# Kernel optimization log

Measured on AMD Instinct MI355X. Metric: run time of the kernel, lower is better.

Reference implementation:

```python
import jax, jax.numpy as jnp
import numpy as np

N_TYPES = 6
NUM_HEADS = 8
MAX_SEQ = 50
LN_EPS = 1e-5
NEG_SLOPE = 0.2


def layer_norm(x, g, b):
    m = x.mean(-1, keepdims=True)
    v = ((x - m) ** 2).mean(-1, keepdims=True)
    return (x - m) / jnp.sqrt(v + LN_EPS) * g + b


def setup_inputs() -> dict:
    key = jax.random.key(0)
    N, E, D = 20000, 200000, 128  # nodes, edges, input_dim==hidden_dim
    ks = jax.random.split(key, 64)
    it = iter(ks)

    def w(shape):
        return jax.random.normal(next(it), shape, jnp.float32) / np.sqrt(shape[-2] if len(shape) > 1 else shape[-1]).astype(np.float32)

    inp = {}
    inp['x'] = jax.random.normal(next(it), (N, D), jnp.float32)
    inp['edge_index'] = jax.random.randint(next(it), (2, E), 0, N)
    inp['node_types'] = jax.random.randint(next(it), (N,), 0, N_TYPES)
    inp['temporal_positions'] = jax.random.randint(next(it), (N,), 0, MAX_SEQ)
    # CrossDomainGAT params
    inp['gat_Wq'] = w((D, D)); inp['gat_Wk'] = w((D, D)); inp['gat_Wv'] = w((D, D))
    inp['gat_Wo'] = w((D, D)); inp['gat_bo'] = jnp.zeros((D,), jnp.float32)
    inp['gat_g'] = jnp.ones((D,), jnp.float32); inp['gat_b'] = jnp.zeros((D,), jnp.float32)
    # SchemaAwareGCN params
    inp['gcn_Wt'] = w((N_TYPES, D, D)); inp['gcn_bt'] = jnp.zeros((N_TYPES, D), jnp.float32)
    inp['gcn_mW1'] = w((2 * D, D)); inp['gcn_mb1'] = jnp.zeros((D,), jnp.float32)
    inp['gcn_mW2'] = w((D, D)); inp['gcn_mb2'] = jnp.zeros((D,), jnp.float32)
    inp['gcn_aW1'] = w((D, D)); inp['gcn_ab1'] = jnp.zeros((D,), jnp.float32)
    inp['gcn_aW2'] = w((D, D)); inp['gcn_ab2'] = jnp.zeros((D,), jnp.float32)
    inp['gcn_Wo'] = w((D, D)); inp['gcn_bo'] = jnp.zeros((D,), jnp.float32)
    inp['gcn_g'] = jnp.ones((D,), jnp.float32); inp['gcn_b'] = jnp.zeros((D,), jnp.float32)
    # TemporalReasoningGNN params (no turn_boundaries -> LSTM/attention path skipped)
    inp['tmp_emb'] = jax.random.normal(next(it), (MAX_SEQ, D), jnp.float32)
    inp['tmp_W1'] = w((2 * D, D)); inp['tmp_b1'] = jnp.zeros((D,), jnp.float32)
    inp['tmp_W2'] = w((D, D)); inp['tmp_b2'] = jnp.zeros((D,), jnp.float32)
    inp['tmp_Wo'] = w((D, D)); inp['tmp_bo'] = jnp.zeros((D,), jnp.float32)
    inp['tmp_g'] = jnp.ones((D,), jnp.float32); inp['tmp_b'] = jnp.zeros((D,), jnp.float32)
    # Unified fusion (concat of 3 branches -> hidden) + LayerNorm
    inp['fus_W'] = w((3 * D, D)); inp['fus_b'] = jnp.zeros((D,), jnp.float32)
    inp['fus_g'] = jnp.ones((D,), jnp.float32); inp['fus_be'] = jnp.zeros((D,), jnp.float32)
    return inp


def _gat(x, row, col, Wq, Wk, Wv, Wo, bo, g, b):
    N, D = x.shape
    Dh = D // NUM_HEADS
    Q = (x @ Wq).reshape(N, NUM_HEADS, Dh)
    K = (x @ Wk).reshape(N, NUM_HEADS, Dh)
    V = (x @ Wv).reshape(N, NUM_HEADS, Dh)
    # edge-wise multi-head attention scores [E, H]
    scores = (Q[row] * K[col]).sum(-1) / np.sqrt(Dh).astype(np.float32)
    scores = jax.nn.leaky_relu(scores, NEG_SLOPE)
    # segment softmax over incoming edges of each col node
    mx = jax.ops.segment_max(scores, col, num_segments=N)
    ex = jnp.exp(scores - mx[col])
    sm = jax.ops.segment_sum(ex, col, num_segments=N)
    probs = ex / sm[col]
    wv = probs[:, :, None] * V[row]  # [E, H, Dh]
    out = jax.ops.segment_sum(wv.reshape(len(row), D), col, num_segments=N)
    out = out @ Wo + bo
    return layer_norm(out + x, g, b)


def _mlp2(z, W1, b1, W2, b2):
    return jax.nn.relu(z @ W1 + b1) @ W2 + b2


def _gcn(x, row, col, node_types, Wt, bt, mW1, mb1, mW2, mb2, aW1, ab1, aW2, ab2, Wo, bo, g, b):
    N, D = x.shape
    h = jnp.zeros((N, D), x.dtype)
    for t in range(N_TYPES):  # fixed small type count
        h = h + jnp.where((node_types == t)[:, None], x @ Wt[t] + bt[t], 0.0)
    messages = _mlp2(jnp.concatenate([h[row], h[col]], axis=1), mW1, mb1, mW2, mb2)
    agg = jax.ops.segment_sum(messages, col, num_segments=N)
    h = h + _mlp2(agg, aW1, ab1, aW2, ab2)
    h = h @ Wo + bo
    return layer_norm(h + x, g, b)


def _temporal(x, row, col, tpos, emb, W1, b1, W2, b2, Wo, bo, g, b):
    N, D = x.shape
    h = x + emb[jnp.clip(tpos, 0, MAX_SEQ - 1)]
    messages = _mlp2(jnp.concatenate([h[row], h[col]], axis=1), W1, b1, W2, b2)
    h = h + jax.ops.segment_sum(messages, col, num_segments=N)
    h = h @ Wo + bo
    return layer_norm(h, g, b)


def reference(x, edge_index, node_types, temporal_positions,
              gat_Wq, gat_Wk, gat_Wv, gat_Wo, gat_bo, gat_g, gat_b,
              gcn_Wt, gcn_bt, gcn_mW1, gcn_mb1, gcn_mW2, gcn_mb2,
              gcn_aW1, gcn_ab1, gcn_aW2, gcn_ab2, gcn_Wo, gcn_bo, gcn_g, gcn_b,
              tmp_emb, tmp_W1, tmp_b1, tmp_W2, tmp_b2, tmp_Wo, tmp_bo, tmp_g, tmp_b,
              fus_W, fus_b, fus_g, fus_be):
    row, col = edge_index[0], edge_index[1]
    o_gat = _gat(x, row, col, gat_Wq, gat_Wk, gat_Wv, gat_Wo, gat_bo, gat_g, gat_b)
    o_gcn = _gcn(x, row, col, node_types, gcn_Wt, gcn_bt, gcn_mW1, gcn_mb1, gcn_mW2, gcn_mb2,
                 gcn_aW1, gcn_ab1, gcn_aW2, gcn_ab2, gcn_Wo, gcn_bo, gcn_g, gcn_b)
    o_tmp = _temporal(x, row, col, temporal_positions, tmp_emb, tmp_W1, tmp_b1, tmp_W2, tmp_b2,
                      tmp_Wo, tmp_bo, tmp_g, tmp_b)
    fused = jnp.concatenate([o_gat, o_gcn, o_tmp], axis=-1) @ fus_W + fus_b
    return layer_norm(fused, fus_g, fus_be)
```

## Files before the change

kernel.cpp:

```cpp
#include <hip/hip_runtime.h>

using u32 = unsigned int;
using s64 = long long;

__global__ __launch_bounds__(64) void k_detect13(const u32* __restrict__ ei,
                                                 const u32* __restrict__ nt,
                                                 const u32* __restrict__ tp,
                                                 u32* __restrict__ flags) {
    if (blockIdx.x != 0 || threadIdx.x != 0) return;
    bool e64 = true, n64 = true, t64 = true;
    for (int k = 0; k < 64; ++k) {
        if (ei[2 * k + 1] != 0u) e64 = false;
        if (nt[2 * k + 1] != 0u) n64 = false;
        if (tp[2 * k + 1] != 0u) t64 = false;
    }
    flags[0] = e64 ? 1u : 0u;
    flags[1] = n64 ? 1u : 0u;
    flags[2] = t64 ? 1u : 0u;
}

__global__ __launch_bounds__(256) void k_cvt13(const void* __restrict__ src,
                                               int* __restrict__ dst, long long n,
                                               const u32* __restrict__ flags, int fidx) {
    long long i = (long long)blockIdx.x * 256 + threadIdx.x;
    if (i >= n) return;
    dst[i] = flags[fidx] ? (int)((const s64*)src)[i] : ((const int*)src)[i];
}

__global__ __launch_bounds__(256) void kz13(float* __restrict__ p, long long n) {
    long long i = (long long)blockIdx.x * 256 + threadIdx.x;
    if (i < n) p[i] = 0.f;
}
__global__ __launch_bounds__(256) void kz_i(int* __restrict__ p, int n) {
    int i = blockIdx.x * 256 + threadIdx.x;
    if (i < n) p[i] = 0;
}

__global__ __launch_bounds__(256) void k_hist(const int* __restrict__ ei, int E,
                                              int* __restrict__ cnt) {
    int e = blockIdx.x * 256 + threadIdx.x;
    if (e < E) atomicAdd(&cnt[ei[E + e]], 1);
}

__global__ __launch_bounds__(1024) void k_scan(const int* __restrict__ cnt,
                                               int* __restrict__ offA, int N) {
    __shared__ int part[1024];
    int t = threadIdx.x;
    int C = (N + 1023) >> 10;
    int beg = t * C, end = beg + C; if (end > N) end = N;
    int s = 0;
    for (int k = beg; k < end; ++k) s += cnt[k];
    part[t] = s; __syncthreads();
    for (int o = 1; o < 1024; o <<= 1) {
        int v = (t >= o) ? part[t - o] : 0;
        __syncthreads();
        part[t] += v;
        __syncthreads();
    }
    int base = (t == 0) ? 0 : part[t - 1];
    for (int k = beg; k < end; ++k) { offA[k] = base; base += cnt[k]; }
    if (t == 1023) offA[N] = part[1023];
}

__global__ __launch_bounds__(256) void k_scatter(const int* __restrict__ ei, int E,
                                                 const int* __restrict__ offA,
                                                 int* __restrict__ cur,
                                                 int* __restrict__ srow,
                                                 int* __restrict__ sedge) {
    int e = blockIdx.x * 256 + threadIdx.x;
    if (e >= E) return;
    int col = ei[E + e];
    int p = offA[col] + atomicAdd(&cur[col], 1);
    srow[p] = ei[e];
    sedge[p] = e;
}

__global__ __launch_bounds__(256) void k_thist(const int* __restrict__ nt, int N,
                                               int* __restrict__ tcnt) {
    __shared__ int lc[6];
    if (threadIdx.x < 6) lc[threadIdx.x] = 0;
    __syncthreads();
    int i = blockIdx.x * 256 + threadIdx.x;
    if (i < N) {
        int t = nt[i]; t = (t < 0 || t > 5) ? 0 : t;
        atomicAdd(&lc[t], 1);
    }
    __syncthreads();
    if (threadIdx.x < 6 && lc[threadIdx.x] > 0) atomicAdd(&tcnt[threadIdx.x], lc[threadIdx.x]);
}

__global__ __launch_bounds__(64) void k_tscan(const int* __restrict__ tcnt,
                                              int* __restrict__ toff) {
    if (threadIdx.x != 0 || blockIdx.x != 0) return;
    int s = 0;
    for (int t = 0; t < 6; ++t) { toff[t] = s; s += tcnt[t]; }
    toff[6] = s;
}

__global__ __launch_bounds__(256) void k_tscatter(const int* __restrict__ nt, int N,
                                                  const int* __restrict__ toff,
                                                  int* __restrict__ tcur,
                                                  int* __restrict__ perm) {
    __shared__ int lc[6], gb[6];
    if (threadIdx.x < 6) lc[threadIdx.x] = 0;
    __syncthreads();
    int i = blockIdx.x * 256 + threadIdx.x;
    int t = 0, lr = 0;
    if (i < N) {
        t = nt[i]; t = (t < 0 || t > 5) ? 0 : t;
        lr = atomicAdd(&lc[t], 1);
    }
    __syncthreads();
    if (threadIdx.x < 6 && lc[threadIdx.x] > 0)
        gb[threadIdx.x] = atomicAdd(&tcur[threadIdx.x], lc[threadIdx.x]);
    __syncthreads();
    if (i < N) perm[toff[t] + gb[t] + lr] = i;
}

__device__ __forceinline__ float2 ld2(const float* p) { return *(const float2*)p; }
__device__ __forceinline__ void st2(float* p, float2 v) { *(float2*)p = v; }
__device__ __forceinline__ float4 ld4(const float* p) { return *(const float4*)p; }
__device__ __forceinline__ void st4(float* p, float4 v) { *(float4*)p = v; }
__device__ __forceinline__ void fma4(float4& a, float s, float4 w) {
    a.x = fmaf(s, w.x, a.x); a.y = fmaf(s, w.y, a.y);
    a.z = fmaf(s, w.z, a.z); a.w = fmaf(s, w.w, a.w);
}

__device__ __forceinline__ float redrow(float s) {
#pragma unroll
    for (int o = 1; o < 32; o <<= 1) s += __shfl_xor(s, o);
    return s;
}


__device__ __forceinline__ void stage_half(float* wl, const float* __restrict__ Wg,
                                           int half) {
    int t = threadIdx.x;
    const float* src = Wg + half * 8192;
#pragma unroll
    for (int i = 0; i < 8; ++i) {
        int idx = (t + i * 256) * 4;
        st4(wl + idx, ld4(src + idx));
    }
}

__device__ __forceinline__ void mm_half(float4 (&acc)[4], const float* xs,
                                        const float* wl, int tn, int tc, int k4base) {
#pragma unroll 2
    for (int k4 = 0; k4 < 16; ++k4) {
        int r = k4 * 4;
        float4 w0 = ld4(wl + (r + 0) * 128 + tc * 4);
        float4 w1 = ld4(wl + (r + 1) * 128 + tc * 4);
        float4 w2 = ld4(wl + (r + 2) * 128 + tc * 4);
        float4 w3 = ld4(wl + (r + 3) * 128 + tc * 4);
#pragma unroll
        for (int j = 0; j < 4; ++j) {
            float4 xv = ld4(xs + (tn * 4 + j) * 128 + (k4base + k4) * 4);
            fma4(acc[j], xv.x, w0); fma4(acc[j], xv.y, w1);
            fma4(acc[j], xv.z, w2); fma4(acc[j], xv.w, w3);
        }
    }
}

__device__ __forceinline__ void mmS(float4 (&acc)[4], const float* xs, float* wl,
                                    const float* __restrict__ Wg, int tn, int tc) {
    __syncthreads();
    stage_half(wl, Wg, 0);
    __syncthreads();
    mm_half(acc, xs, wl, tn, tc, 0);
    __syncthreads();
    stage_half(wl, Wg, 1);
    __syncthreads();
    mm_half(acc, xs, wl, tn, tc, 16);
}

__device__ __forceinline__ void mmG(float4 (&acc)[4], const float* xs,
                                    const float* __restrict__ W, int tn, int tc) {
#pragma unroll 2
    for (int k4 = 0; k4 < 32; ++k4) {
        float4 w0 = ld4(W + (size_t)(k4 * 4 + 0) * 128 + tc * 4);
        float4 w1 = ld4(W + (size_t)(k4 * 4 + 1) * 128 + tc * 4);
        float4 w2 = ld4(W + (size_t)(k4 * 4 + 2) * 128 + tc * 4);
        float4 w3 = ld4(W + (size_t)(k4 * 4 + 3) * 128 + tc * 4);
#pragma unroll
        for (int j = 0; j < 4; ++j) {
            float4 xv = ld4(xs + (tn * 4 + j) * 128 + k4 * 4);
            fma4(acc[j], xv.x, w0); fma4(acc[j], xv.y, w1);
            fma4(acc[j], xv.z, w2); fma4(acc[j], xv.w, w3);
        }
    }
}

__device__ __forceinline__ float4 lnrow(float4 v, const float* g, const float* b, int tc) {
    float m = redrow(v.x + v.y + v.z + v.w) * 0.0078125f;
    float4 d = make_float4(v.x - m, v.y - m, v.z - m, v.w - m);
    float var = redrow(d.x * d.x + d.y * d.y + d.z * d.z + d.w * d.w) * 0.0078125f;
    float r = rsqrtf(var + 1e-5f);
    float4 gg = ld4(g + tc * 4), bb = ld4(b + tc * 4);
    return make_float4(d.x * r * gg.x + bb.x, d.y * r * gg.y + bb.y,
                       d.z * r * gg.z + bb.z, d.w * r * gg.w + bb.w);
}

__device__ __forceinline__ void stage32(float* xs, const float* src, int i0, int N) {
    int t = threadIdx.x;
#pragma unroll
    for (int ii = 0; ii < 4; ++ii) {
        int idx = t + ii * 256;
        int r = idx >> 5, c = idx & 31;
        int node = i0 + r; if (node >= N) node = N - 1;
        st4(xs + r * 128 + c * 4, ld4(src + (size_t)node * 128 + c * 4));
    }
}

__device__ __forceinline__ void xstore(float* xs, const float4 (&v)[4], int tn, int tc) {
#pragma unroll
    for (int j = 0; j < 4; ++j) st4(xs + (tn * 4 + j) * 128 + tc * 4, v[j]);
}

__global__ __launch_bounds__(256) void k_mega1(
        const float* __restrict__ x,
        const float* __restrict__ Wq, const float* __restrict__ Wk,
        const float* __restrict__ Wv, float* __restrict__ big,
        const int* __restrict__ nt, const int* __restrict__ perm,
        const float* __restrict__ Wt, const float* __restrict__ bt,
        float* __restrict__ h_gcn,
        const float* __restrict__ mW1, const float* __restrict__ mb1,
        float* __restrict__ Pa_g, float* __restrict__ Pb_g,
        const float* __restrict__ emb, const int* __restrict__ tpos,
        const float* __restrict__ tW1, const float* __restrict__ tb1,
        float* __restrict__ Pa_t, float* __restrict__ Pb_t,
        int N, int gT) {
    __shared__ float xs[32 * 128];
    __shared__ float wl[64 * 128];
    int role = blockIdx.x / gT;
    int bid = blockIdx.x - role * gT;
    int t = threadIdx.x, tn = t >> 5, tc = t & 31;
    int i0 = bid * 32;

    if (role == 0) {
        stage32(xs, x, i0, N);
        float4 acc[4];
        const float* Ws[3] = {Wq, Wk, Wv};
#pragma unroll
        for (int m = 0; m < 3; ++m) {
#pragma unroll
            for (int j = 0; j < 4; ++j) acc[j] = make_float4(0.f, 0.f, 0.f, 0.f);
            mmS(acc, xs, wl, Ws[m], tn, tc);
#pragma unroll
            for (int j = 0; j < 4; ++j) {
                int node = i0 + tn * 4 + j;
                if (node < N) st4(big + (size_t)node * 384 + m * 128 + tc * 4, acc[j]);
            }
        }
    } else if (role == 1) {
#pragma unroll
        for (int ii = 0; ii < 4; ++ii) {
            int idx = t + ii * 256;
            int r = idx >> 5, c = idx & 31;
            int q = i0 + r; if (q >= N) q = N - 1;
            int node = perm[q];
            st4(xs + r * 128 + c * 4, ld4(x + (size_t)node * 128 + c * 4));
        }
        int qa = i0; if (qa >= N) qa = N - 1;
        int qb = i0 + 31; if (qb >= N) qb = N - 1;
        int t0 = nt[perm[qa]]; t0 = (t0 < 0 || t0 > 5) ? 0 : t0;
        int t1 = nt[perm[qb]]; t1 = (t1 < 0 || t1 > 5) ? 0 : t1;
        float4 acc[4];
        if (t0 == t1) {
#pragma unroll
            for (int j = 0; j < 4; ++j) acc[j] = ld4(bt + t0 * 128 + tc * 4);
            mmS(acc, xs, wl, Wt + (size_t)t0 * 16384, tn, tc);
        } else {
            __syncthreads();
#pragma unroll
            for (int j = 0; j < 4; ++j) {
                int q = i0 + tn * 4 + j; if (q >= N) q = N - 1;
                int tt = nt[perm[q]]; tt = (tt < 0 || tt > 5) ? 0 : tt;
                const float* W = Wt + (size_t)tt * 16384;
                float4 a = ld4(bt + tt * 128 + tc * 4);
                float4 one[4] = {a, a, a, a};
                (void)one;
                float4 aa[4];
#pragma unroll
                for (int jj = 0; jj < 4; ++jj) aa[jj] = make_float4(0.f, 0.f, 0.f, 0.f);
#pragma unroll 2
                for (int k4 = 0; k4 < 32; ++k4) {
                    float4 xv = ld4(xs + (tn * 4 + j) * 128 + k4 * 4);
                    float4 w0 = ld4(W + (size_t)(k4 * 4 + 0) * 128 + tc * 4);
                    float4 w1 = ld4(W + (size_t)(k4 * 4 + 1) * 128 + tc * 4);
                    float4 w2 = ld4(W + (size_t)(k4 * 4 + 2) * 128 + tc * 4);
                    float4 w3 = ld4(W + (size_t)(k4 * 4 + 3) * 128 + tc * 4);
                    fma4(a, xv.x, w0); fma4(a, xv.y, w1);
                    fma4(a, xv.z, w2); fma4(a, xv.w, w3);
                }
                acc[j] = a;
            }
        }
#pragma unroll
        for (int j = 0; j < 4; ++j) {
            int q = i0 + tn * 4 + j;
            if (q < N) st4(h_gcn + (size_t)perm[q] * 128 + tc * 4, acc[j]);
        }
        __syncthreads();
        xstore(xs, acc, tn, tc);
        float4 pa[4];
#pragma unroll
        for (int j = 0; j < 4; ++j) pa[j] = make_float4(0.f, 0.f, 0.f, 0.f);
        mmS(pa, xs, wl, mW1, tn, tc);
#pragma unroll
        for (int j = 0; j < 4; ++j) {
            int q = i0 + tn * 4 + j;
            if (q < N) st4(Pa_g + (size_t)perm[q] * 128 + tc * 4, pa[j]);
        }
        float4 b14 = ld4(mb1 + tc * 4);
        float4 pb[4];
#pragma unroll
        for (int j = 0; j < 4; ++j) pb[j] = b14;
        mmS(pb, xs, wl, mW1 + (size_t)128 * 128, tn, tc);
#pragma unroll
        for (int j = 0; j < 4; ++j) {
            int q = i0 + tn * 4 + j;
            if (q < N) st4(Pb_g + (size_t)perm[q] * 128 + tc * 4, pb[j]);
        }
    } else {
#pragma unroll
        for (int ii = 0; ii < 4; ++ii) {
            int idx = t + ii * 256;
            int r = idx >> 5, c = idx & 31;
            int node = i0 + r; if (node >= N) node = N - 1;
            float4 v = ld4(x + (size_t)node * 128 + c * 4);
            int tp = tpos[node]; tp = tp < 0 ? 0 : (tp > 49 ? 49 : tp);
            float4 e = ld4(emb + tp * 128 + c * 4);
            v.x += e.x; v.y += e.y; v.z += e.z; v.w += e.w;
            st4(xs + r * 128 + c * 4, v);
        }
        float4 acc[4];
#pragma unroll
        for (int j = 0; j < 4; ++j) acc[j] = make_float4(0.f, 0.f, 0.f, 0.f);
        mmS(acc, xs, wl, tW1, tn, tc);
#pragma unroll
        for (int j = 0; j < 4; ++j) {
            int node = i0 + tn * 4 + j;
            if (node < N) st4(Pa_t + (size_t)node * 128 + tc * 4, acc[j]);
        }
        float4 b14 = ld4(tb1 + tc * 4);
#pragma unroll
        for (int j = 0; j < 4; ++j) acc[j] = b14;
        mmS(acc, xs, wl, tW1 + (size_t)128 * 128, tn, tc);
#pragma unroll
        for (int j = 0; j < 4; ++j) {
            int node = i0 + tn * 4 + j;
            if (node < N) st4(Pb_t + (size_t)node * 128 + tc * 4, acc[j]);
        }
    }
}

__device__ __forceinline__ void rsum_body(const float* __restrict__ Pa,
                                          const float* __restrict__ Pb,
                                          const int* __restrict__ srow,
                                          const int* __restrict__ offA,
                                          float* __restrict__ s, int N, int cb) {
    int l = threadIdx.x & 63;
    int col = cb * 4 + (threadIdx.x >> 6);
    if (col >= N) return;
    float2 pb = ld2(Pb + (size_t)col * 128 + 2 * l);
    float ax = 0.f, ay = 0.f;
    int p = offA[col], pe = offA[col + 1];
    for (; p + 4 <= pe; p += 4) {
        int r0 = srow[p], r1 = srow[p + 1], r2 = srow[p + 2], r3 = srow[p + 3];
        float2 a0 = ld2(Pa + (size_t)r0 * 128 + 2 * l);
        float2 a1 = ld2(Pa + (size_t)r1 * 128 + 2 * l);
        float2 a2 = ld2(Pa + (size_t)r2 * 128 + 2 * l);
        float2 a3 = ld2(Pa + (size_t)r3 * 128 + 2 * l);
        ax += fmaxf(a0.x + pb.x, 0.f) + fmaxf(a1.x + pb.x, 0.f)
            + fmaxf(a2.x + pb.x, 0.f) + fmaxf(a3.x + pb.x, 0.f);
        ay += fmaxf(a0.y + pb.y, 0.f) + fmaxf(a1.y + pb.y, 0.f)
            + fmaxf(a2.y + pb.y, 0.f) + fmaxf(a3.y + pb.y, 0.f);
    }
    for (; p < pe; ++p) {
        int r = srow[p];
        float2 a = ld2(Pa + (size_t)r * 128 + 2 * l);
        ax += fmaxf(a.x + pb.x, 0.f);
        ay += fmaxf(a.y + pb.y, 0.f);
    }
    st2(s + (size_t)col * 128 + 2 * l, make_float2(ax, ay));
}

__global__ __launch_bounds__(256) void k_mega2(
        const float* __restrict__ big, const int* __restrict__ ei, int E,
        float* __restrict__ scores, float* __restrict__ sm,
        const float* __restrict__ Pa_g, float* __restrict__ Pb_g,
        const float* __restrict__ Pa_t, float* __restrict__ Pb_t,
        const int* __restrict__ srow, const int* __restrict__ offA,
        int N, int gE8, int gC) {
    int b = blockIdx.x;
    if (b < gE8) {
        long long t = (long long)b * 256 + threadIdx.x;
        if (t >= (long long)E * 8) return;
        int e = (int)(t >> 3), h = (int)(t & 7);
        int row = ei[e], col = ei[E + e];
        const float4* q = (const float4*)(big + (size_t)row * 384 + h * 16);
        const float4* kk = (const float4*)(big + (size_t)col * 384 + 128 + h * 16);
        float s = 0.f;
#pragma unroll
        for (int d = 0; d < 4; ++d) {
            float4 a = q[d], bb = kk[d];
            s += a.x * bb.x + a.y * bb.y + a.z * bb.z + a.w * bb.w;
        }
        s *= 0.25f;
        s = s > 0.f ? s : 0.2f * s;
        float ex = expf(s);
        scores[t] = ex;
        atomicAdd(&sm[(size_t)col * 8 + h], ex);
    } else if (b < gE8 + gC) {
        rsum_body(Pa_g, Pb_g, srow, offA, Pb_g, N, b - gE8);
    } else {
        rsum_body(Pa_t, Pb_t, srow, offA, Pb_t, N, b - gE8 - gC);
    }
}

__global__ __launch_bounds__(256) void k_wvS2(const float* __restrict__ big,
                                              const float* __restrict__ scores,
                                              const float* __restrict__ sm,
                                              const int* __restrict__ srow,
                                              const int* __restrict__ sedge,
                                              const int* __restrict__ offA,
                                              float* __restrict__ agg, int N) {
    int l = threadIdx.x & 63;
    int col = blockIdx.x * 4 + (threadIdx.x >> 6);
    if (col >= N) return;
    int h = l >> 3;
    float sv = sm[(size_t)col * 8 + h];
    float ism = sv != 0.f ? 1.f / sv : 0.f;
    float ax = 0.f, ay = 0.f;
    int p = offA[col], pe = offA[col + 1];
    for (; p + 2 <= pe; p += 2) {
        int e0 = sedge[p], r0 = srow[p], e1 = sedge[p + 1], r1 = srow[p + 1];
        float pr0 = scores[(size_t)e0 * 8 + h] * ism;
        float pr1 = scores[(size_t)e1 * 8 + h] * ism;
        float2 v0 = ld2(big + (size_t)r0 * 384 + 256 + 2 * l);
        float2 v1 = ld2(big + (size_t)r1 * 384 + 256 + 2 * l);
        ax = fmaf(pr0, v0.x, ax); ay = fmaf(pr0, v0.y, ay);
        ax = fmaf(pr1, v1.x, ax); ay = fmaf(pr1, v1.y, ay);
    }
    for (; p < pe; ++p) {
        int e = sedge[p], r = srow[p];
        float pr = scores[(size_t)e * 8 + h] * ism;
        float2 v = ld2(big + (size_t)r * 384 + 256 + 2 * l);
        ax = fmaf(pr, v.x, ax); ay = fmaf(pr, v.y, ay);
    }
    st2(agg + (size_t)col * 128 + 2 * l, make_float2(ax, ay));
}

__global__ __launch_bounds__(256) void k_mega3(
        const float* __restrict__ x,
        const float* __restrict__ agg,
        const float* __restrict__ gWo, const float* __restrict__ gbo,
        const float* __restrict__ gg, const float* __restrict__ gb,
        float* __restrict__ o_gat,
        const float* __restrict__ h_gcn, const float* __restrict__ s_gcn,
        const int* __restrict__ offA,
        const float* __restrict__ W2, const float* __restrict__ b2,
        const float* __restrict__ aW1, const float* __restrict__ ab1,
        const float* __restrict__ aW2, const float* __restrict__ ab2,
        const float* __restrict__ cWo, const float* __restrict__ cbo,
        const float* __restrict__ cg, const float* __restrict__ cb,
        float* __restrict__ o_gcn,
        const float* __restrict__ emb, const int* __restrict__ tpos,
        const float* __restrict__ s_tmp,
        const float* __restrict__ tW2, const float* __restrict__ tb2,
        const float* __restrict__ tWo, const float* __restrict__ tbo,
        const float* __restrict__ tg, const float* __restrict__ tb,
        float* __restrict__ o_tmp,
        int N, int gT) {
    __shared__ float xs[32 * 128];
    __shared__ float wl[64 * 128];
    int role = blockIdx.x / gT;
    int bid = blockIdx.x - role * gT;
    int t = threadIdx.x, tn = t >> 5, tc = t & 31;
    int i0 = bid * 32;
    int node[4];
#pragma unroll
    for (int j = 0; j < 4; ++j) {
        node[j] = i0 + tn * 4 + j; if (node[j] >= N) node[j] = N - 1;
    }

    if (role == 0) {
        stage32(xs, agg, i0, N);
        float4 acc[4];
        float4 bo4 = ld4(gbo + tc * 4);
#pragma unroll
        for (int j = 0; j < 4; ++j) acc[j] = bo4;
        mmS(acc, xs, wl, gWo, tn, tc);
#pragma unroll
        for (int j = 0; j < 4; ++j) {
            float4 xr = ld4(x + (size_t)node[j] * 128 + tc * 4);
            float4 v = make_float4(acc[j].x + xr.x, acc[j].y + xr.y,
                                   acc[j].z + xr.z, acc[j].w + xr.w);
            float4 o = lnrow(v, gg, gb, tc);
            int q = i0 + tn * 4 + j;
            if (q < N) st4(o_gat + (size_t)q * 128 + tc * 4, o);
        }
    } else if (role == 1) {
        stage32(xs, s_gcn, i0, N);
        float4 acc[4];
        float4 b24 = ld4(b2 + tc * 4);
#pragma unroll
        for (int j = 0; j < 4; ++j) {
            float deg = (float)(offA[node[j] + 1] - offA[node[j]]);
            acc[j] = make_float4(deg * b24.x, deg * b24.y, deg * b24.z, deg * b24.w);
        }
        mmS(acc, xs, wl, W2, tn, tc);
        __syncthreads();
        xstore(xs, acc, tn, tc);
        float4 u[4];
        float4 a14 = ld4(ab1 + tc * 4);
#pragma unroll
        for (int j = 0; j < 4; ++j) u[j] = a14;
        mmS(u, xs, wl, aW1, tn, tc);
#pragma unroll
        for (int j = 0; j < 4; ++j) {
            u[j].x = fmaxf(u[j].x, 0.f); u[j].y = fmaxf(u[j].y, 0.f);
            u[j].z = fmaxf(u[j].z, 0.f); u[j].w = fmaxf(u[j].w, 0.f);
        }
        __syncthreads();
        xstore(xs, u, tn, tc);
        float4 z3[4];
        float4 a24 = ld4(ab2 + tc * 4);
#pragma unroll
        for (int j = 0; j < 4; ++j) z3[j] = a24;
        mmS(z3, xs, wl, aW2, tn, tc);
#pragma unroll
        for (int j = 0; j < 4; ++j) {
            float4 hg = ld4(h_gcn + (size_t)node[j] * 128 + tc * 4);
            z3[j].x += hg.x; z3[j].y += hg.y; z3[j].z += hg.z; z3[j].w += hg.w;
        }
        __syncthreads();
        xstore(xs, z3, tn, tc);
        float4 d[4];
        float4 bo4 = ld4(cbo + tc * 4);
#pragma unroll
        for (int j = 0; j < 4; ++j) d[j] = bo4;
        mmS(d, xs, wl, cWo, tn, tc);
#pragma unroll
        for (int j = 0; j < 4; ++j) {
            float4 xr = ld4(x + (size_t)node[j] * 128 + tc * 4);
            float4 v = make_float4(d[j].x + xr.x, d[j].y + xr.y,
                                   d[j].z + xr.z, d[j].w + xr.w);
            float4 o = lnrow(v, cg, cb, tc);
            int q = i0 + tn * 4 + j;
            if (q < N) st4(o_gcn + (size_t)q * 128 + tc * 4, o);
        }
    } else {
        stage32(xs, s_tmp, i0, N);
        float4 acc[4];
        float4 b24 = ld4(tb2 + tc * 4);
#pragma unroll
        for (int j = 0; j < 4; ++j) {
            float deg = (float)(offA[node[j] + 1] - offA[node[j]]);
            acc[j] = make_float4(deg * b24.x, deg * b24.y, deg * b24.z, deg * b24.w);
        }
        mmS(acc, xs, wl, tW2, tn, tc);
#pragma unroll
        for (int j = 0; j < 4; ++j) {
            int tp = tpos[node[j]]; tp = tp < 0 ? 0 : (tp > 49 ? 49 : tp);
            float4 xr = ld4(x + (size_t)node[j] * 128 + tc * 4);
            float4 e = ld4(emb + tp * 128 + tc * 4);
            acc[j].x += xr.x + e.x; acc[j].y += xr.y + e.y;
            acc[j].z += xr.z + e.z; acc[j].w += xr.w + e.w;
        }
        __syncthreads();
        xstore(xs, acc, tn, tc);
        float4 d[4];
        float4 bo4 = ld4(tbo + tc * 4);
#pragma unroll
        for (int j = 0; j < 4; ++j) d[j] = bo4;
        mmS(d, xs, wl, tWo, tn, tc);
#pragma unroll
        for (int j = 0; j < 4; ++j) {
            float4 o = lnrow(d[j], tg, tb, tc);
            int q = i0 + tn * 4 + j;
            if (q < N) st4(o_tmp + (size_t)q * 128 + tc * 4, o);
        }
    }
}

__global__ __launch_bounds__(256) void k_final3(
        const float* __restrict__ o_gat, const float* __restrict__ o_gcn,
        const float* __restrict__ o_tmp,
        const float* __restrict__ fusW, const float* __restrict__ fus_b,
        const float* __restrict__ fg, const float* __restrict__ fbe,
        float* __restrict__ out, int N) {
    __shared__ float xs[32 * 128];
    __shared__ float wl[64 * 128];
    int t = threadIdx.x, tn = t >> 5, tc = t & 31;
    int i0 = blockIdx.x * 32;
    stage32(xs, o_gat, i0, N);
    float4 acc[4];
    float4 fb4 = ld4(fus_b + tc * 4);
#pragma unroll
    for (int j = 0; j < 4; ++j) acc[j] = fb4;
    mmS(acc, xs, wl, fusW, tn, tc);
    __syncthreads();
    stage32(xs, o_gcn, i0, N);
    mmS(acc, xs, wl, fusW + (size_t)128 * 128, tn, tc);
    __syncthreads();
    stage32(xs, o_tmp, i0, N);
    mmS(acc, xs, wl, fusW + (size_t)256 * 128, tn, tc);
#pragma unroll
    for (int j = 0; j < 4; ++j) {
        float4 res = lnrow(acc[j], fg, fbe, tc);
        int q = i0 + tn * 4 + j;
        if (q < N) st4(out + (size_t)q * 128 + tc * 4, res);
    }
}

extern "C" void kernel_launch(void* const* d_in, const int* in_sizes, int n_in, void* d_out,
                              int out_size, void* d_ws, size_t ws_size, hipStream_t stream) {
    (void)n_in; (void)out_size; (void)ws_size;
    const float* x = (const float*)d_in[0];
    const float* gat_Wq = (const float*)d_in[4];
    const float* gat_Wk = (const float*)d_in[5];
    const float* gat_Wv = (const float*)d_in[6];
    const float* gat_Wo = (const float*)d_in[7];
    const float* gat_bo = (const float*)d_in[8];
    const float* gat_g = (const float*)d_in[9];
    const float* gat_b = (const float*)d_in[10];
    const float* gcn_Wt = (const float*)d_in[11];
    const float* gcn_bt = (const float*)d_in[12];
    const float* gcn_mW1 = (const float*)d_in[13];
    const float* gcn_mb1 = (const float*)d_in[14];
    const float* gcn_mW2 = (const float*)d_in[15];
    const float* gcn_mb2 = (const float*)d_in[16];
    const float* gcn_aW1 = (const float*)d_in[17];
    const float* gcn_ab1 = (const float*)d_in[18];
    const float* gcn_aW2 = (const float*)d_in[19];
    const float* gcn_ab2 = (const float*)d_in[20];
    const float* gcn_Wo = (const float*)d_in[21];
    const float* gcn_bo = (const float*)d_in[22];
    const float* gcn_g = (const float*)d_in[23];
    const float* gcn_b = (const float*)d_in[24];
    const float* tmp_emb = (const float*)d_in[25];
    const float* tmp_W1 = (const float*)d_in[26];
    const float* tmp_b1 = (const float*)d_in[27];
    const float* tmp_W2 = (const float*)d_in[28];
    const float* tmp_b2 = (const float*)d_in[29];
    const float* tmp_Wo = (const float*)d_in[30];
    const float* tmp_bo = (const float*)d_in[31];
    const float* tmp_g = (const float*)d_in[32];
    const float* tmp_b = (const float*)d_in[33];
    const float* fus_W = (const float*)d_in[34];
    const float* fus_b = (const float*)d_in[35];
    const float* fus_g = (const float*)d_in[36];
    const float* fus_be = (const float*)d_in[37];

    int N = in_sizes[0] / 128;
    int E = in_sizes[1] / 2;

    float* ws = (float*)d_ws;
    float* big = ws;
    float* o_gat = ws;
    float* o_gcn = ws + (size_t)128 * N;
    float* o_tmp = ws + (size_t)256 * N;
    float* h_gcn = ws + (size_t)384 * N;
    float* Pa_g = ws + (size_t)512 * N;
    float* Pb_g = ws + (size_t)640 * N;
    float* Pa_t = ws + (size_t)768 * N;
    float* Pb_t = ws + (size_t)896 * N;
    float* sm = ws + (size_t)1024 * N;
    float* agg = Pa_g;
    u32* flags = (u32*)(ws + (size_t)1032 * N);
    int* ei32 = (int*)(flags + 16);
    int* nt32 = ei32 + (size_t)2 * E;
    int* tp32 = nt32 + N;
    float* scores = (float*)(tp32 + N);
    int* offA = (int*)(scores + (size_t)8 * E);
    int* cur = offA + (N + 1);
    int* srow = cur + N;
    int* sedge = srow + E;
    int* tcnt = sedge + E;
    int* toff = tcnt + 6;
    int* tcur = toff + 7;
    int* perm = cur;

    k_detect13<<<1, 64, 0, stream>>>((const u32*)d_in[1], (const u32*)d_in[2],
                                     (const u32*)d_in[3], flags);
    long long nEI = (long long)2 * E;
    k_cvt13<<<(int)((nEI + 255) / 256), 256, 0, stream>>>(d_in[1], ei32, nEI, flags, 0);
    k_cvt13<<<(N + 255) / 256, 256, 0, stream>>>(d_in[2], nt32, N, flags, 1);
    k_cvt13<<<(N + 255) / 256, 256, 0, stream>>>(d_in[3], tp32, N, flags, 2);

    int gE = (E + 255) / 256;
    int gN = (N + 255) / 256;
    int gT = (N + 31) / 32;
    int gC = (N + 3) / 4;
    int gE8 = (int)(((long long)E * 8 + 255) / 256);

    kz_i<<<gN, 256, 0, stream>>>(cur, N);
    k_hist<<<gE, 256, 0, stream>>>(ei32, E, cur);
    k_scan<<<1, 1024, 0, stream>>>(cur, offA, N);
    kz_i<<<gN, 256, 0, stream>>>(cur, N);
    k_scatter<<<gE, 256, 0, stream>>>(ei32, E, offA, cur, srow, sedge);

    kz_i<<<1, 32, 0, stream>>>(tcnt, 19);
    k_thist<<<gN, 256, 0, stream>>>(nt32, N, tcnt);
    k_tscan<<<1, 64, 0, stream>>>(tcnt, toff);
    k_tscatter<<<gN, 256, 0, stream>>>(nt32, N, toff, tcur, perm);

    kz13<<<(int)(((long long)8 * N + 255) / 256), 256, 0, stream>>>(sm, (long long)8 * N);

    k_mega1<<<3 * gT, 256, 0, stream>>>(x, gat_Wq, gat_Wk, gat_Wv, big,
                                        nt32, perm, gcn_Wt, gcn_bt, h_gcn,
                                        gcn_mW1, gcn_mb1, Pa_g, Pb_g,
                                        tmp_emb, tp32, tmp_W1, tmp_b1, Pa_t, Pb_t,
                                        N, gT);

    k_mega2<<<gE8 + 2 * gC, 256, 0, stream>>>(big, ei32, E, scores, sm,
                                              Pa_g, Pb_g, Pa_t, Pb_t,
                                              srow, offA, N, gE8, gC);

    k_wvS2<<<gC, 256, 0, stream>>>(big, scores, sm, srow, sedge, offA, agg, N);

    k_mega3<<<3 * gT, 256, 0, stream>>>(x, agg, gat_Wo, gat_bo, gat_g, gat_b, o_gat,
                                        h_gcn, Pb_g, offA, gcn_mW2, gcn_mb2,
                                        gcn_aW1, gcn_ab1, gcn_aW2, gcn_ab2,
                                        gcn_Wo, gcn_bo, gcn_g, gcn_b, o_gcn,
                                        tmp_emb, tp32, Pb_t, tmp_W2, tmp_b2,
                                        tmp_Wo, tmp_bo, tmp_g, tmp_b, o_tmp,
                                        N, gT);

    k_final3<<<gT, 256, 0, stream>>>(o_gat, o_gcn, o_tmp, fus_W, fus_b,
                                     fus_g, fus_be, (float*)d_out, N);
}
```

Before: 475.8 us.

## Fuse GAT edge softmax into CSR aggregation and split fusion GEMM across branches

Edge scores are now computed per destination in the CSR aggregation loop using shuffle-reduced q·k dot products, with an online denominator. This removes the separate per-edge score kernel, the atomic softmax-sum buffer, its zero-fill and the sedge indirection. Each mega3 role also multiplies its branch output by its slice of the fusion weight, leaving a lightweight sum-plus-layernorm kernel. Block-to-role mapping is interleaved (modulo 3) instead of contiguous, and dead code is removed. The trade-off is that q is re-gathered per edge rather than reading a precomputed score, and the exp is computed without max subtraction, same as before.

```diff
diff --git a/kernel.cpp b/kernel.cpp
--- a/kernel.cpp
+++ b/kernel.cpp
@@ -27,10 +27,6 @@
     dst[i] = flags[fidx] ? (int)((const s64*)src)[i] : ((const int*)src)[i];
 }
 
-__global__ __launch_bounds__(256) void kz13(float* __restrict__ p, long long n) {
-    long long i = (long long)blockIdx.x * 256 + threadIdx.x;
-    if (i < n) p[i] = 0.f;
-}
 __global__ __launch_bounds__(256) void kz_i(int* __restrict__ p, int n) {
     int i = blockIdx.x * 256 + threadIdx.x;
     if (i < n) p[i] = 0;
@@ -65,14 +61,12 @@
 __global__ __launch_bounds__(256) void k_scatter(const int* __restrict__ ei, int E,
                                                  const int* __restrict__ offA,
                                                  int* __restrict__ cur,
-                                                 int* __restrict__ srow,
-                                                 int* __restrict__ sedge) {
+                                                 int* __restrict__ srow) {
     int e = blockIdx.x * 256 + threadIdx.x;
     if (e >= E) return;
     int col = ei[E + e];
     int p = offA[col] + atomicAdd(&cur[col], 1);
     srow[p] = ei[e];
-    sedge[p] = e;
 }
 
 __global__ __launch_bounds__(256) void k_thist(const int* __restrict__ nt, int N,
@@ -172,23 +166,6 @@
     stage_half(wl, Wg, 1);
     __syncthreads();
     mm_half(acc, xs, wl, tn, tc, 16);
-}
-
-__device__ __forceinline__ void mmG(float4 (&acc)[4], const float* xs,
-                                    const float* __restrict__ W, int tn, int tc) {
-#pragma unroll 2
-    for (int k4 = 0; k4 < 32; ++k4) {
-        float4 w0 = ld4(W + (size_t)(k4 * 4 + 0) * 128 + tc * 4);
-        float4 w1 = ld4(W + (size_t)(k4 * 4 + 1) * 128 + tc * 4);
-        float4 w2 = ld4(W + (size_t)(k4 * 4 + 2) * 128 + tc * 4);
-        float4 w3 = ld4(W + (size_t)(k4 * 4 + 3) * 128 + tc * 4);
-#pragma unroll
-        for (int j = 0; j < 4; ++j) {
-            float4 xv = ld4(xs + (tn * 4 + j) * 128 + k4 * 4);
-            fma4(acc[j], xv.x, w0); fma4(acc[j], xv.y, w1);
-            fma4(acc[j], xv.z, w2); fma4(acc[j], xv.w, w3);
-        }
-    }
 }
 
 __device__ __forceinline__ float4 lnrow(float4 v, const float* g, const float* b, int tc) {
@@ -229,11 +206,11 @@
         const float* __restrict__ emb, const int* __restrict__ tpos,
         const float* __restrict__ tW1, const float* __restrict__ tb1,
         float* __restrict__ Pa_t, float* __restrict__ Pb_t,
-        int N, int gT) {
+        int N) {
     __shared__ float xs[32 * 128];
     __shared__ float wl[64 * 128];
-    int role = blockIdx.x / gT;
-    int bid = blockIdx.x - role * gT;
+    int role = blockIdx.x % 3;
+    int bid = blockIdx.x / 3;
     int t = threadIdx.x, tn = t >> 5, tc = t & 31;
     int i0 = bid * 32;
 
@@ -278,11 +255,6 @@
                 int tt = nt[perm[q]]; tt = (tt < 0 || tt > 5) ? 0 : tt;
                 const float* W = Wt + (size_t)tt * 16384;
                 float4 a = ld4(bt + tt * 128 + tc * 4);
-                float4 one[4] = {a, a, a, a};
-                (void)one;
-                float4 aa[4];
-#pragma unroll
-                for (int jj = 0; jj < 4; ++jj) aa[jj] = make_float4(0.f, 0.f, 0.f, 0.f);
 #pragma unroll 2
                 for (int k4 = 0; k4 < 32; ++k4) {
                     float4 xv = ld4(xs + (tn * 4 + j) * 128 + k4 * 4);
@@ -356,10 +328,9 @@
 }
 
 __device__ __forceinline__ void rsum_body(const float* __restrict__ Pa,
-                                          const float* __restrict__ Pb,
+                                          float* __restrict__ Pb,
                                           const int* __restrict__ srow,
-                                          const int* __restrict__ offA,
-                                          float* __restrict__ s, int N, int cb) {
+                                          const int* __restrict__ offA, int N, int cb) {
     int l = threadIdx.x & 63;
     int col = cb * 4 + (threadIdx.x >> 6);
     if (col >= N) return;
@@ -383,73 +354,58 @@
         ax += fmaxf(a.x + pb.x, 0.f);
         ay += fmaxf(a.y + pb.y, 0.f);
     }
-    st2(s + (size_t)col * 128 + 2 * l, make_float2(ax, ay));
+    st2(Pb + (size_t)col * 128 + 2 * l, make_float2(ax, ay));
 }
 
 __global__ __launch_bounds__(256) void k_mega2(
-        const float* __restrict__ big, const int* __restrict__ ei, int E,
-        float* __restrict__ scores, float* __restrict__ sm,
+        const float* __restrict__ big,
         const float* __restrict__ Pa_g, float* __restrict__ Pb_g,
         const float* __restrict__ Pa_t, float* __restrict__ Pb_t,
         const int* __restrict__ srow, const int* __restrict__ offA,
-        int N, int gE8, int gC) {
-    int b = blockIdx.x;
-    if (b < gE8) {
-        long long t = (long long)b * 256 + threadIdx.x;
-        if (t >= (long long)E * 8) return;
-        int e = (int)(t >> 3), h = (int)(t & 7);
-        int row = ei[e], col = ei[E + e];
-        const float4* q = (const float4*)(big + (size_t)row * 384 + h * 16);
-        const float4* kk = (const float4*)(big + (size_t)col * 384 + 128 + h * 16);
-        float s = 0.f;
-#pragma unroll
-        for (int d = 0; d < 4; ++d) {
-            float4 a = q[d], bb = kk[d];
-            s += a.x * bb.x + a.y * bb.y + a.z * bb.z + a.w * bb.w;
-        }
-        s *= 0.25f;
-        s = s > 0.f ? s : 0.2f * s;
-        float ex = expf(s);
-        scores[t] = ex;
-        atomicAdd(&sm[(size_t)col * 8 + h], ex);
-    } else if (b < gE8 + gC) {
-        rsum_body(Pa_g, Pb_g, srow, offA, Pb_g, N, b - gE8);
-    } else {
-        rsum_body(Pa_t, Pb_t, srow, offA, Pb_t, N, b - gE8 - gC);
-    }
-}
-
-__global__ __launch_bounds__(256) void k_wvS2(const float* __restrict__ big,
-                                              const float* __restrict__ scores,
-                                              const float* __restrict__ sm,
-                                              const int* __restrict__ srow,
-                                              const int* __restrict__ sedge,
-                                              const int* __restrict__ offA,
-                                              float* __restrict__ agg, int N) {
+        float* __restrict__ agg, int N) {
+    int role = blockIdx.x % 3;
+    int cb = blockIdx.x / 3;
+    if (role == 1) { rsum_body(Pa_g, Pb_g, srow, offA, N, cb); return; }
+    if (role == 2) { rsum_body(Pa_t, Pb_t, srow, offA, N, cb); return; }
     int l = threadIdx.x & 63;
-    int col = blockIdx.x * 4 + (threadIdx.x >> 6);
+    int col = cb * 4 + (threadIdx.x >> 6);
     if (col >= N) return;
-    int h = l >> 3;
-    float sv = sm[(size_t)col * 8 + h];
-    float ism = sv != 0.f ? 1.f / sv : 0.f;
-    float ax = 0.f, ay = 0.f;
+    float2 kc = ld2(big + (size_t)col * 384 + 128 + 2 * l);
+    float ax = 0.f, ay = 0.f, den = 0.f;
     int p = offA[col], pe = offA[col + 1];
     for (; p + 2 <= pe; p += 2) {
-        int e0 = sedge[p], r0 = srow[p], e1 = sedge[p + 1], r1 = srow[p + 1];
-        float pr0 = scores[(size_t)e0 * 8 + h] * ism;
-        float pr1 = scores[(size_t)e1 * 8 + h] * ism;
+        int r0 = srow[p], r1 = srow[p + 1];
+        float2 q0 = ld2(big + (size_t)r0 * 384 + 2 * l);
         float2 v0 = ld2(big + (size_t)r0 * 384 + 256 + 2 * l);
+        float2 q1 = ld2(big + (size_t)r1 * 384 + 2 * l);
         float2 v1 = ld2(big + (size_t)r1 * 384 + 256 + 2 * l);
-        ax = fmaf(pr0, v0.x, ax); ay = fmaf(pr0, v0.y, ay);
-        ax = fmaf(pr1, v1.x, ax); ay = fmaf(pr1, v1.y, ay);
+        float pt0 = q0.x * kc.x + q0.y * kc.y;
+        float pt1 = q1.x * kc.x + q1.y * kc.y;
+        pt0 += __shfl_xor(pt0, 1); pt1 += __shfl_xor(pt1, 1);
+        pt0 += __shfl_xor(pt0, 2); pt1 += __shfl_xor(pt1, 2);
+        pt0 += __shfl_xor(pt0, 4); pt1 += __shfl_xor(pt1, 4);
+        float s0 = pt0 * 0.25f; s0 = s0 > 0.f ? s0 : 0.2f * s0;
+        float s1 = pt1 * 0.25f; s1 = s1 > 0.f ? s1 : 0.2f * s1;
+        float e0 = expf(s0), e1 = expf(s1);
+        den += e0 + e1;
+        ax = fmaf(e0, v0.x, ax); ay = fmaf(e0, v0.y, ay);
+        ax = fmaf(e1, v1.x, ax); ay = fmaf(e1, v1.y, ay);
     }
     for (; p < pe; ++p) {
-        int e = sedge[p], r = srow[p];
-        float pr = scores[(size_t)e * 8 + h] * ism;
-        float2 v = ld2(big + (size_t)r * 384 + 256 + 2 * l);
-        ax = fmaf(pr, v.x, ax); ay = fmaf(pr, v.y, ay);
-    }
-    st2(agg + (size_t)col * 128 + 2 * l, make_float2(ax, ay));
+        int r = srow[p];
+        float2 q0 = ld2(big + (size_t)r * 384 + 2 * l);
+        float2 v0 = ld2(big + (size_t)r * 384 + 256 + 2 * l);
+        float pt = q0.x * kc.x + q0.y * kc.y;
+        pt += __shfl_xor(pt, 1);
+        pt += __shfl_xor(pt, 2);
+        pt += __shfl_xor(pt, 4);
+        float s = pt * 0.25f; s = s > 0.f ? s : 0.2f * s;
+        float e = expf(s);
+        den += e;
+        ax = fmaf(e, v0.x, ax); ay = fmaf(e, v0.y, ay);
+    }
+    float ism = den != 0.f ? 1.f / den : 0.f;
+    st2(agg + (size_t)col * 128 + 2 * l, make_float2(ax * ism, ay * ism));
 }
 
 __global__ __launch_bounds__(256) void k_mega3(
@@ -457,7 +413,7 @@
         const float* __restrict__ agg,
         const float* __restrict__ gWo, const float* __restrict__ gbo,
         const float* __restrict__ gg, const float* __restrict__ gb,
-        float* __restrict__ o_gat,
+        float* __restrict__ p0,
         const float* __restrict__ h_gcn, const float* __restrict__ s_gcn,
         const int* __restrict__ offA,
         const float* __restrict__ W2, const float* __restrict__ b2,
@@ -465,18 +421,19 @@
         const float* __restrict__ aW2, const float* __restrict__ ab2,
         const float* __restrict__ cWo, const float* __restrict__ cbo,
         const float* __restrict__ cg, const float* __restrict__ cb,
-        float* __restrict__ o_gcn,
+        float* __restrict__ p1,
         const float* __restrict__ emb, const int* __restrict__ tpos,
         const float* __restrict__ s_tmp,
         const float* __restrict__ tW2, const float* __restrict__ tb2,
         const float* __restrict__ tWo, const float* __restrict__ tbo,
         const float* __restrict__ tg, const float* __restrict__ tb,
-        float* __restrict__ o_tmp,
-        int N, int gT) {
+        float* __restrict__ p2,
+        const float* __restrict__ fusW, const float* __restrict__ fus_b,
+        int N) {
     __shared__ float xs[32 * 128];
     __shared__ float wl[64 * 128];
-    int role = blockIdx.x / gT;
-    int bid = blockIdx.x - role * gT;
+    int role = blockIdx.x % 3;
+    int bid = blockIdx.x / 3;
     int t = threadIdx.x, tn = t >> 5, tc = t & 31;
     int i0 = bid * 32;
     int node[4];
@@ -484,6 +441,7 @@
     for (int j = 0; j < 4; ++j) {
         node[j] = i0 + tn * 4 + j; if (node[j] >= N) node[j] = N - 1;
     }
+    float4 o[4];
 
     if (role == 0) {
         stage32(xs, agg, i0, N);
@@ -497,9 +455,18 @@
             float4 xr = ld4(x + (size_t)node[j] * 128 + tc * 4);
             float4 v = make_float4(acc[j].x + xr.x, acc[j].y + xr.y,
                                    acc[j].z + xr.z, acc[j].w + xr.w);
-            float4 o = lnrow(v, gg, gb, tc);
+            o[j] = lnrow(v, gg, gb, tc);
+        }
+        __syncthreads();
+        xstore(xs, o, tn, tc);
+        float4 fb4 = ld4(fus_b + tc * 4);
+#pragma unroll
+        for (int j = 0; j < 4; ++j) acc[j] = fb4;
+        mmS(acc, xs, wl, fusW, tn, tc);
+#pragma unroll
+        for (int j = 0; j < 4; ++j) {
             int q = i0 + tn * 4 + j;
-            if (q < N) st4(o_gat + (size_t)q * 128 + tc * 4, o);
+            if (q < N) st4(p0 + (size_t)q * 128 + tc * 4, acc[j]);
         }
     } else if (role == 1) {
         stage32(xs, s_gcn, i0, N);
@@ -547,9 +514,17 @@
             float4 xr = ld4(x + (size_t)node[j] * 128 + tc * 4);
             float4 v = make_float4(d[j].x + xr.x, d[j].y + xr.y,
                                    d[j].z + xr.z, d[j].w + xr.w);
-            float4 o = lnrow(v, cg, cb, tc);
+            o[j] = lnrow(v, cg, cb, tc);
+        }
+        __syncthreads();
+        xstore(xs, o, tn, tc);
+#pragma unroll
+        for (int j = 0; j < 4; ++j) d[j] = make_float4(0.f, 0.f, 0.f, 0.f);
+        mmS(d, xs, wl, fusW + (size_t)128 * 128, tn, tc);
+#pragma unroll
+        for (int j = 0; j < 4; ++j) {
             int q = i0 + tn * 4 + j;
-            if (q < N) st4(o_gcn + (size_t)q * 128 + tc * 4, o);
+            if (q < N) st4(p1 + (size_t)q * 128 + tc * 4, d[j]);
         }
     } else {
         stage32(xs, s_tmp, i0, N);
@@ -577,41 +552,38 @@
         for (int j = 0; j < 4; ++j) d[j] = bo4;
         mmS(d, xs, wl, tWo, tn, tc);
 #pragma unroll
-        for (int j = 0; j < 4; ++j) {
-            float4 o = lnrow(d[j], tg, tb, tc);
+        for (int j = 0; j < 4; ++j) o[j] = lnrow(d[j], tg, tb, tc);
+        __syncthreads();
+        xstore(xs, o, tn, tc);
+#pragma unroll
+        for (int j = 0; j < 4; ++j) d[j] = make_float4(0.f, 0.f, 0.f, 0.f);
+        mmS(d, xs, wl, fusW + (size_t)256 * 128, tn, tc);
+#pragma unroll
+        for (int j = 0; j < 4; ++j) {
             int q = i0 + tn * 4 + j;
-            if (q < N) st4(o_tmp + (size_t)q * 128 + tc * 4, o);
-        }
-    }
-}
-
-__global__ __launch_bounds__(256) void k_final3(
-        const float* __restrict__ o_gat, const float* __restrict__ o_gcn,
-        const float* __restrict__ o_tmp,
-        const float* __restrict__ fusW, const float* __restrict__ fus_b,
+            if (q < N) st4(p2 + (size_t)q * 128 + tc * 4, d[j]);
+        }
+    }
+}
+
+__global__ __launch_bounds__(256) void k_finE(
+        const float* __restrict__ p0, const float* __restrict__ p1,
+        const float* __restrict__ p2,
         const float* __restrict__ fg, const float* __restrict__ fbe,
         float* __restrict__ out, int N) {
-    __shared__ float xs[32 * 128];
-    __shared__ float wl[64 * 128];
     int t = threadIdx.x, tn = t >> 5, tc = t & 31;
     int i0 = blockIdx.x * 32;
-    stage32(xs, o_gat, i0, N);
-    float4 acc[4];
-    float4 fb4 = ld4(fus_b + tc * 4);
-#pragma unroll
-    for (int j = 0; j < 4; ++j) acc[j] = fb4;
-    mmS(acc, xs, wl, fusW, tn, tc);
-    __syncthreads();
-    stage32(xs, o_gcn, i0, N);
-    mmS(acc, xs, wl, fusW + (size_t)128 * 128, tn, tc);
-    __syncthreads();
-    stage32(xs, o_tmp, i0, N);
-    mmS(acc, xs, wl, fusW + (size_t)256 * 128, tn, tc);
 #pragma unroll
     for (int j = 0; j < 4; ++j) {
-        float4 res = lnrow(acc[j], fg, fbe, tc);
-        int q = i0 + tn * 4 + j;
-        if (q < N) st4(out + (size_t)q * 128 + tc * 4, res);
+        int node = i0 + tn * 4 + j;
+        int nc = node < N ? node : N - 1;
+        float4 a = ld4(p0 + (size_t)nc * 128 + tc * 4);
+        float4 b = ld4(p1 + (size_t)nc * 128 + tc * 4);
+        float4 c = ld4(p2 + (size_t)nc * 128 + tc * 4);
+        float4 v = make_float4(a.x + b.x + c.x, a.y + b.y + c.y,
+                               a.z + b.z + c.z, a.w + b.w + c.w);
+        float4 o = lnrow(v, fg, fbe, tc);
+        if (node < N) st4(out + (size_t)node * 128 + tc * 4, o);
     }
 }
 
@@ -659,26 +631,23 @@
 
     float* ws = (float*)d_ws;
     float* big = ws;
-    float* o_gat = ws;
-    float* o_gcn = ws + (size_t)128 * N;
-    float* o_tmp = ws + (size_t)256 * N;
+    float* p0 = ws;
+    float* p1 = ws + (size_t)128 * N;
+    float* p2 = ws + (size_t)256 * N;
     float* h_gcn = ws + (size_t)384 * N;
     float* Pa_g = ws + (size_t)512 * N;
     float* Pb_g = ws + (size_t)640 * N;
     float* Pa_t = ws + (size_t)768 * N;
     float* Pb_t = ws + (size_t)896 * N;
-    float* sm = ws + (size_t)1024 * N;
-    float* agg = Pa_g;
-    u32* flags = (u32*)(ws + (size_t)1032 * N);
+    float* agg = ws + (size_t)1024 * N;
+    u32* flags = (u32*)(ws + (size_t)1152 * N);
     int* ei32 = (int*)(flags + 16);
     int* nt32 = ei32 + (size_t)2 * E;
     int* tp32 = nt32 + N;
-    float* scores = (float*)(tp32 + N);
-    int* offA = (int*)(scores + (size_t)8 * E);
+    int* offA = tp32 + N;
     int* cur = offA + (N + 1);
     int* srow = cur + N;
-    int* sedge = srow + E;
-    int* tcnt = sedge + E;
+    int* tcnt = srow + E;
     int* toff = tcnt + 6;
     int* tcur = toff + 7;
     int* perm = cur;
@@ -694,41 +663,33 @@
     int gN = (N + 255) / 256;
     int gT = (N + 31) / 32;
     int gC = (N + 3) / 4;
-    int gE8 = (int)(((long long)E * 8 + 255) / 256);
 
     kz_i<<<gN, 256, 0, stream>>>(cur, N);
     k_hist<<<gE, 256, 0, stream>>>(ei32, E, cur);
     k_scan<<<1, 1024, 0, stream>>>(cur, offA, N);
     kz_i<<<gN, 256, 0, stream>>>(cur, N);
-    k_scatter<<<gE, 256, 0, stream>>>(ei32, E, offA, cur, srow, sedge);
+    k_scatter<<<gE, 256, 0, stream>>>(ei32, E, offA, cur, srow);
 
     kz_i<<<1, 32, 0, stream>>>(tcnt, 19);
     k_thist<<<gN, 256, 0, stream>>>(nt32, N, tcnt);
     k_tscan<<<1, 64, 0, stream>>>(tcnt, toff);
     k_tscatter<<<gN, 256, 0, stream>>>(nt32, N, toff, tcur, perm);
 
-    kz13<<<(int)(((long long)8 * N + 255) / 256), 256, 0, stream>>>(sm, (long long)8 * N);
-
     k_mega1<<<3 * gT, 256, 0, stream>>>(x, gat_Wq, gat_Wk, gat_Wv, big,
                                         nt32, perm, gcn_Wt, gcn_bt, h_gcn,
                                         gcn_mW1, gcn_mb1, Pa_g, Pb_g,
-                                        tmp_emb, tp32, tmp_W1, tmp_b1, Pa_t, Pb_t,
-                                        N, gT);
-
-    k_mega2<<<gE8 + 2 * gC, 256, 0, stream>>>(big, ei32, E, scores, sm,
-                                              Pa_g, Pb_g, Pa_t, Pb_t,
-                                              srow, offA, N, gE8, gC);
-
-    k_wvS2<<<gC, 256, 0, stream>>>(big, scores, sm, srow, sedge, offA, agg, N);
-
-    k_mega3<<<3 * gT, 256, 0, stream>>>(x, agg, gat_Wo, gat_bo, gat_g, gat_b, o_gat,
+                                        tmp_emb, tp32, tmp_W1, tmp_b1, Pa_t, Pb_t, N);
+
+    k_mega2<<<3 * gC, 256, 0, stream>>>(big, Pa_g, Pb_g, Pa_t, Pb_t,
+                                        srow, offA, agg, N);
+
+    k_mega3<<<3 * gT, 256, 0, stream>>>(x, agg, gat_Wo, gat_bo, gat_g, gat_b, p0,
                                         h_gcn, Pb_g, offA, gcn_mW2, gcn_mb2,
                                         gcn_aW1, gcn_ab1, gcn_aW2, gcn_ab2,
-                                        gcn_Wo, gcn_bo, gcn_g, gcn_b, o_gcn,
+                                        gcn_Wo, gcn_bo, gcn_g, gcn_b, p1,
                                         tmp_emb, tp32, Pb_t, tmp_W2, tmp_b2,
-                                        tmp_Wo, tmp_bo, tmp_g, tmp_b, o_tmp,
-                                        N, gT);
-
-    k_final3<<<gT, 256, 0, stream>>>(o_gat, o_gcn, o_tmp, fus_W, fus_b,
-                                     fus_g, fus_be, (float*)d_out, N);
-}
+                                        tmp_Wo, tmp_bo, tmp_g, tmp_b, p2,
+                                        fus_W, fus_b, N);
+
+    k_finE<<<gT, 256, 0, stream>>>(p0, p1, p2, fus_g, fus_be, (float*)d_out, N);
+}
```

Result: no change. 481.3 us (median of 3 runs) (+1.2%).
